# Kernel tuning notes

Hardware: AMD Instinct MI355X
Metric: run time of the kernel (lower is better)

Reference implementation:

```python
import jax, jax.numpy as jnp
import numpy as np

S, P = 64, 32          # scenes, pedestrians per scene (uniform)
N = S * P              # total pedestrians = 2048
H, E = 64, 64          # h_dim, embedding_dim
D1, D2 = 512, 1024     # mlp_pre_pool hidden, bottleneck_dim
EPS = 1e-5             # torch BatchNorm1d eps


def _batchnorm(x, gamma, beta):
    # Training-mode BN with per-scene batch stats (matches the per-scene
    # loop in the original, where BN sees one scene's num_ped^2 rows).
    # x: [S, P*P, D]
    mu = jnp.mean(x, axis=1, keepdims=True)
    var = jnp.mean(jnp.square(x - mu), axis=1, keepdims=True)  # biased var, as torch BN
    return (x - mu) * jax.lax.rsqrt(var + EPS) * gamma + beta


def setup_inputs() -> dict:
    key = jax.random.key(0)
    ks = jax.random.split(key, 16)
    h_states = jax.random.normal(ks[0], (1, N, H), jnp.float32)
    starts = jnp.arange(S, dtype=jnp.int32) * P
    seq_start_end = jnp.stack([starts, starts + P], axis=1)  # [S, 2]
    end_pos = jax.random.normal(ks[1], (N, 2), jnp.float32)
    rel_pos = jax.random.normal(ks[2], (N, 2), jnp.float32)  # unused (pooling_dim=2) but a fwd arg
    sc = 0.05
    params = dict(
        W_embed=jax.random.normal(ks[3], (2, E), jnp.float32) * sc,
        b_embed=jnp.zeros((E,), jnp.float32),
        W1=jax.random.normal(ks[4], (E + H, D1), jnp.float32) * sc,
        b1=jnp.zeros((D1,), jnp.float32),
        g1=jnp.ones((D1,), jnp.float32),
        be1=jnp.zeros((D1,), jnp.float32),
        W2=jax.random.normal(ks[5], (D1, D2), jnp.float32) * sc,
        b2=jnp.zeros((D2,), jnp.float32),
        g2=jnp.ones((D2,), jnp.float32),
        be2=jnp.zeros((D2,), jnp.float32),
    )
    return dict(h_states=h_states, seq_start_end=seq_start_end,
                end_pos=end_pos, rel_pos=rel_pos, **params)


def reference(h_states, seq_start_end, end_pos, rel_pos,
              W_embed, b_embed, W1, b1, g1, be1, W2, b2, g2, be2):
    # Uniform scenes: seq_start_end delimits S contiguous blocks of P peds.
    pos = end_pos.reshape(S, P, 2)
    h = h_states.reshape(N, H).reshape(S, P, H)
    # Original indexing: row (k*P + j) -> pos[j] - pos[k], hidden[j];
    # the final view(P, P, -1).max(1) maxes over j for each k.
    rel = pos[:, None, :, :] - pos[:, :, None, :]          # [S, Pk, Pj, 2]
    emb = rel @ W_embed + b_embed                          # [S, Pk, Pj, E]
    hid = jnp.broadcast_to(h[:, None, :, :], (S, P, P, H)) # hidden of j
    x = jnp.concatenate([emb, hid], axis=-1).reshape(S, P * P, E + H)
    x = jax.nn.relu(_batchnorm(x @ W1 + b1, g1, be1))      # [S, P*P, 512]
    x = jax.nn.relu(_batchnorm(x @ W2 + b2, g2, be2))      # [S, P*P, 1024]
    pool_h = x.reshape(S, P, P, D2).max(axis=2)            # max over j
    return pool_h.reshape(N, D2)
```

## Files before the change

### kernel.cpp

```cpp
#include <hip/hip_runtime.h>
#include <hip/hip_bf16.h>

#define S_ 64
#define P_ 32
#define N_ 2048
#define H_ 64
#define E_ 64
#define D1_ 512
#define D2_ 1024
#define EPS_ 1e-5f

typedef unsigned short u16;
using bf16x8 = __attribute__((ext_vector_type(8))) __bf16;
using floatx4 = __attribute__((ext_vector_type(4))) float;

__device__ inline u16 f2bf(float x) {
    unsigned u = __float_as_uint(x);
    unsigned r = (u + 0x7fffu + ((u >> 16) & 1u)) >> 16;
    return (u16)r;
}


__device__ void prep_scene_256(int u, int tid, float* smem,
                               const float* __restrict__ pos, const float* __restrict__ h,
                               const float* __restrict__ We, const float* __restrict__ W1,
                               const float* __restrict__ g1, const float* __restrict__ be1,
                               float* __restrict__ A, float* __restrict__ Bv) {
    const int s = u >> 2, dq = u & 3;
    const int jg = tid >> 7, dl = tid & 127;
    const int d = (dq << 7) + dl;
    float* hs = smem;
    float* ps = smem + 2048;
    float* red = smem + 2112;
    for (int i = tid; i < 2048; i += 256) hs[i] = h[(size_t)s * 2048 + i];
    if (tid < 64) ps[tid] = pos[s * 64 + tid];
    __syncthreads();
    float wq0 = 0.f, wq1 = 0.f;
    for (int e = 0; e < 64; ++e) {
        const float wv = W1[e * 512 + d];
        wq0 += We[e] * wv;
        wq1 += We[64 + e] * wv;
    }
    float w[16], uu[16];
#pragma unroll
    for (int jj = 0; jj < 16; ++jj) w[jj] = 0.f;
    const float4* h4 = (const float4*)hs;
    for (int e4 = 0; e4 < 16; ++e4) {
        const float c0 = W1[(64 + e4 * 4 + 0) * 512 + d];
        const float c1 = W1[(64 + e4 * 4 + 1) * 512 + d];
        const float c2 = W1[(64 + e4 * 4 + 2) * 512 + d];
        const float c3 = W1[(64 + e4 * 4 + 3) * 512 + d];
#pragma unroll
        for (int jj = 0; jj < 16; ++jj) {
            const float4 hv = h4[((jg << 4) + jj) * 16 + e4];
            w[jj] += hv.x * c0 + hv.y * c1 + hv.z * c2 + hv.w * c3;
        }
    }
    float sw = 0.f, sww = 0.f, su = 0.f, suu = 0.f;
#pragma unroll
    for (int jj = 0; jj < 16; ++jj) {
        const int j = (jg << 4) + jj;
        uu[jj] = ps[2 * j] * wq0 + ps[2 * j + 1] * wq1;
        w[jj] += uu[jj];
        sw += w[jj]; sww += w[jj] * w[jj];
        su += uu[jj]; suu += uu[jj] * uu[jj];
    }
    red[(jg << 7) + dl] = sw;
    red[256 + (jg << 7) + dl] = sww;
    red[512 + (jg << 7) + dl] = su;
    red[768 + (jg << 7) + dl] = suu;
    __syncthreads();
    const float tw = red[dl] + red[128 + dl];
    const float tww = red[256 + dl] + red[384 + dl];
    const float tu = red[512 + dl] + red[640 + dl];
    const float tuu = red[768 + dl] + red[896 + dl];
    const float mw = tw * (1.f / 32.f), mu2 = tu * (1.f / 32.f);
    const float var = (tww * (1.f / 32.f) - mw * mw) + (tuu * (1.f / 32.f) - mu2 * mu2);
    const float sc = rsqrtf(var + EPS_) * g1[d];
    const float bb = be1[d];
#pragma unroll
    for (int jj = 0; jj < 16; ++jj) {
        const int j = (jg << 4) + jj;
        A[(size_t)(s * 32 + j) * 512 + d] = (w[jj] - mw) * sc + bb;
        Bv[(size_t)(s * 32 + j) * 512 + d] = (uu[jj] - mu2) * sc;
    }
}

__device__ void w2t_tile_256(int b2, int tid, void* smem,
                             const float* __restrict__ W2, u16* __restrict__ w2t) {
    float (*tile)[65] = (float (*)[65])smem;
    const int bi = b2 & 15, bj = b2 >> 4;
    const int tx = tid & 63, ty = tid >> 6;
#pragma unroll
    for (int i = 0; i < 64; i += 4)
        tile[ty + i][tx] = W2[(size_t)(bj * 64 + ty + i) * 1024 + bi * 64 + tx];
    __syncthreads();
#pragma unroll
    for (int i = 0; i < 64; i += 4)
        w2t[(size_t)(bi * 64 + ty + i) * 512 + bj * 64 + tx] = f2bf(tile[tx][ty + i]);
}

__global__ __launch_bounds__(256, 2)
void k_gemm(const float* __restrict__ A, const float* __restrict__ Bv,
            const u16* __restrict__ w2t,
            float* __restrict__ maxv, float* __restrict__ minv,
            float* __restrict__ psum, float* __restrict__ psumsq) {
    __shared__ __align__(16) u16 As[128 * 64];
    __shared__ __align__(16) u16 Ws[256 * 64];
    const int tid = threadIdx.x;
    const int wave = tid >> 6, lane = tid & 63;
    const int wm = wave >> 1, wn = wave & 1;
    const int quad = lane >> 4, l16 = lane & 15;
    const int lrow = lane >> 3, lchk = lane & 7;
    const int gchk = lchk ^ lrow;
    const int sj = tid >> 3, sc8 = tid & 7;
    const int mt = blockIdx.x;
    const int s2 = mt >> 3, rb = mt & 7;
    const int pedb = rb << 2;
    const float* Aj = A + ((size_t)(s2 * 32 + sj) << 9) + (sc8 << 3);
    const float* Bp = Bv + ((size_t)(s2 * 32 + pedb) << 9) + (sc8 << 3);
    const int swz = (sc8 ^ (sj & 7)) << 3;

    for (int cs = 0; cs < 4; ++cs) {
        const int N0 = cs << 8;
        floatx4 acc[4][8] = {};
        for (int it = 0; it < 8; ++it) {
            const int k0 = it << 6;
#pragma unroll
            for (int t = 0; t < 8; ++t) {
                const int rbase = (wave << 6) + (t << 3);
                const u16* gb = w2t + (size_t)(N0 + rbase + lrow) * 512 + (k0 + (gchk << 3));
                __builtin_amdgcn_global_load_lds(
                    (const __attribute__((address_space(1))) void*)gb,
                    (__attribute__((address_space(3))) void*)(Ws + (rbase << 6)), 16, 0, 0);
            }
            {
                const float4 alo = *(const float4*)(Aj + k0);
                const float4 ahi = *(const float4*)(Aj + k0 + 4);
#pragma unroll
                for (int p = 0; p < 4; ++p) {
                    const int r = (p << 5) + sj;
                    const float4 blo = *(const float4*)(Bp + ((size_t)p << 9) + k0);
                    const float4 bhi = *(const float4*)(Bp + ((size_t)p << 9) + k0 + 4);
                    bf16x8 o;
                    o[0] = (__bf16)fmaxf(alo.x - blo.x, 0.f);
                    o[1] = (__bf16)fmaxf(alo.y - blo.y, 0.f);
                    o[2] = (__bf16)fmaxf(alo.z - blo.z, 0.f);
                    o[3] = (__bf16)fmaxf(alo.w - blo.w, 0.f);
                    o[4] = (__bf16)fmaxf(ahi.x - bhi.x, 0.f);
                    o[5] = (__bf16)fmaxf(ahi.y - bhi.y, 0.f);
                    o[6] = (__bf16)fmaxf(ahi.z - bhi.z, 0.f);
                    o[7] = (__bf16)fmaxf(ahi.w - bhi.w, 0.f);
                    *(bf16x8*)(As + (r << 6) + swz) = o;
                }
            }
            __syncthreads();
#pragma unroll
            for (int kk = 0; kk < 2; ++kk) {
                const int ck = (kk << 2) + quad;
                const int po = (ck ^ (l16 & 7)) << 3;
                bf16x8 af[4], wf[8];
#pragma unroll
                for (int tm = 0; tm < 4; ++tm) {
                    const int row = (wm << 6) + (tm << 4) + l16;
                    af[tm] = *(const bf16x8*)(As + (row << 6) + po);
                }
#pragma unroll
                for (int tn = 0; tn < 8; ++tn) {
                    const int wrow = (wn << 7) + (tn << 4) + l16;
                    wf[tn] = *(const bf16x8*)(Ws + (wrow << 6) + ((ck ^ (wrow & 7)) << 3));
                }
#pragma unroll
                for (int tm = 0; tm < 4; ++tm)
#pragma unroll
                    for (int tn = 0; tn < 8; ++tn)
                        acc[tm][tn] = __builtin_amdgcn_mfma_f32_16x16x32_bf16(
                            af[tm], wf[tn], acc[tm][tn], 0, 0, 0);
            }
            __syncthreads();
        }
#pragma unroll
        for (int tn = 0; tn < 8; ++tn) {
            const int col = N0 + (wn << 7) + (tn << 4) + l16;
            float wsum = 0.f, wsq = 0.f;
#pragma unroll
            for (int gp = 0; gp < 2; ++gp) {
                float vmax = -3.4e38f, vmin = 3.4e38f, vs = 0.f, vq = 0.f;
#pragma unroll
                for (int tm = gp * 2; tm < gp * 2 + 2; ++tm)
#pragma unroll
                    for (int r = 0; r < 4; ++r) {
                        const float v = acc[tm][tn][r];
                        vmax = fmaxf(vmax, v);
                        vmin = fminf(vmin, v);
                        vs += v;
                        vq += v * v;
                    }
#pragma unroll
                for (int off = 16; off < 64; off <<= 1) {
                    vmax = fmaxf(vmax, __shfl_xor(vmax, off));
                    vmin = fminf(vmin, __shfl_xor(vmin, off));
                    vs += __shfl_xor(vs, off);
                    vq += __shfl_xor(vq, off);
                }
                if (quad == 0) {
                    const int kg = s2 * 32 + pedb + (wm << 1) + gp;
                    maxv[(size_t)kg * 1024 + col] = vmax;
                    minv[(size_t)kg * 1024 + col] = vmin;
                }
                wsum += vs;
                wsq += vq;
            }
            if (quad == 0) {
                const int slot = (s2 << 4) + (rb << 1) + wm;
                psum[(size_t)slot * 1024 + col] = wsum;
                psumsq[(size_t)slot * 1024 + col] = wsq;
            }
        }
    }
}

__global__ __launch_bounds__(256)
void k_prep(const float* __restrict__ pos, const float* __restrict__ h,
            const float* __restrict__ We, const float* __restrict__ W1,
            const float* __restrict__ g1, const float* __restrict__ be1,
            const float* __restrict__ W2,
            float* __restrict__ A, float* __restrict__ Bv, u16* __restrict__ w2t) {
    __shared__ __align__(16) char smem_raw[16912];
    const int bid = blockIdx.x;
    if (bid < 256)
        prep_scene_256(bid, threadIdx.x, (float*)smem_raw, pos, h, We, W1, g1, be1, A, Bv);
    else
        w2t_tile_256(bid - 256, threadIdx.x, smem_raw, W2, w2t);
}

__global__ __launch_bounds__(256)
void k_final(const float* __restrict__ maxv, const float* __restrict__ minv,
             const float* __restrict__ psum, const float* __restrict__ psumsq,
             const float* __restrict__ g2, const float* __restrict__ be2,
             float* __restrict__ out) {
    const int u = blockIdx.x, tid = threadIdx.x;
    const int s3 = u >> 2;
    const int c = ((u & 3) << 8) + tid;
    float sm = 0.f, sq = 0.f;
#pragma unroll
    for (int t = 0; t < 16; ++t) {
        sm += psum[(size_t)(s3 * 16 + t) * 1024 + c];
        sq += psumsq[(size_t)(s3 * 16 + t) * 1024 + c];
    }
    const float mu = sm * (1.f / 1024.f);
    const float var = sq * (1.f / 1024.f) - mu * mu;
    const float inv = rsqrtf(var + EPS_);
    const float scale = g2[c] * inv;
    const float bb = be2[c];
    const float* src = (scale >= 0.f) ? maxv : minv;
    for (int k = 0; k < 32; ++k) {
        const float v = src[(size_t)(s3 * 32 + k) * 1024 + c];
        out[(size_t)(s3 * 32 + k) * 1024 + c] = fmaxf((v - mu) * scale + bb, 0.f);
    }
}

extern "C" void kernel_launch(void* const* d_in, const int* in_sizes, int n_in,
                              void* d_out, int out_size, void* d_ws, size_t ws_size,
                              hipStream_t stream) {
    const float* h_states = (const float*)d_in[0];
    const float* end_pos = (const float*)d_in[2];
    const float* W_embed = (const float*)d_in[4];
    const float* W1 = (const float*)d_in[6];
    const float* g1 = (const float*)d_in[8];
    const float* be1 = (const float*)d_in[9];
    const float* W2 = (const float*)d_in[10];
    const float* g2 = (const float*)d_in[12];
    const float* be2 = (const float*)d_in[13];
    float* out = (float*)d_out;

    float* Abuf = (float*)d_ws;
    float* Bbuf = Abuf + 1048576;
    float* maxv = Bbuf + 1048576;
    float* minv = maxv + 2097152;
    float* psum = minv + 2097152;
    float* psumsq = psum + 1048576;
    u16* w2t = (u16*)(psumsq + 1048576);

    k_prep<<<dim3(384), dim3(256), 0, stream>>>(end_pos, h_states, W_embed, W1,
                                                g1, be1, W2, Abuf, Bbuf, w2t);
    k_gemm<<<dim3(512), dim3(256), 0, stream>>>(Abuf, Bbuf, w2t, maxv, minv, psum, psumsq);
    k_final<<<dim3(256), dim3(256), 0, stream>>>(maxv, minv, psum, psumsq, g2, be2, out);
}
```

Before: 183.9 us.

## Fuse BN2 finalize into GEMM kernel via per-scene last-block counter

Removes the separate k_final launch. Each GEMM block bumps an atomic per-scene counter, and the last of the 8 blocks for a scene reduces the partial sums, applies BN and ReLU, and writes the output. The partial stores become agent-scope atomics so the last block sees them, and a memset is added to reset the counters. The B-tile loads are also hoisted ahead of the conversion loop. In exchange, the tail work is serialized onto the last block of each scene and an extra memset is issued.

```diff
diff --git a/kernel.cpp b/kernel.cpp
--- a/kernel.cpp
+++ b/kernel.cpp
@@ -19,7 +19,6 @@
     unsigned r = (u + 0x7fffu + ((u >> 16) & 1u)) >> 16;
     return (u16)r;
 }
-
 
 __device__ void prep_scene_256(int u, int tid, float* smem,
                                const float* __restrict__ pos, const float* __restrict__ h,
@@ -100,13 +99,31 @@
         w2t[(size_t)(bi * 64 + ty + i) * 512 + bj * 64 + tx] = f2bf(tile[tx][ty + i]);
 }
 
+__global__ __launch_bounds__(256)
+void k_prep(const float* __restrict__ pos, const float* __restrict__ h,
+            const float* __restrict__ We, const float* __restrict__ W1,
+            const float* __restrict__ g1, const float* __restrict__ be1,
+            const float* __restrict__ W2,
+            float* __restrict__ A, float* __restrict__ Bv, u16* __restrict__ w2t) {
+    __shared__ __align__(16) char smem_raw[16912];
+    const int bid = blockIdx.x;
+    if (bid < 256)
+        prep_scene_256(bid, threadIdx.x, (float*)smem_raw, pos, h, We, W1, g1, be1, A, Bv);
+    else
+        w2t_tile_256(bid - 256, threadIdx.x, smem_raw, W2, w2t);
+}
+
 __global__ __launch_bounds__(256, 2)
 void k_gemm(const float* __restrict__ A, const float* __restrict__ Bv,
             const u16* __restrict__ w2t,
             float* __restrict__ maxv, float* __restrict__ minv,
-            float* __restrict__ psum, float* __restrict__ psumsq) {
+            float* __restrict__ psum, float* __restrict__ psumsq,
+            int* __restrict__ cnt,
+            const float* __restrict__ g2, const float* __restrict__ be2,
+            float* __restrict__ out) {
     __shared__ __align__(16) u16 As[128 * 64];
     __shared__ __align__(16) u16 Ws[256 * 64];
+    __shared__ int last_flag;
     const int tid = threadIdx.x;
     const int wave = tid >> 6, lane = tid & 63;
     const int wm = wave >> 1, wn = wave & 1;
@@ -135,22 +152,26 @@
                     (__attribute__((address_space(3))) void*)(Ws + (rbase << 6)), 16, 0, 0);
             }
             {
-                const float4 alo = *(const float4*)(Aj + k0);
-                const float4 ahi = *(const float4*)(Aj + k0 + 4);
+                const float4 a0 = *(const float4*)(Aj + k0);
+                const float4 a1 = *(const float4*)(Aj + k0 + 4);
+                float4 bl[4], bh[4];
+#pragma unroll
+                for (int p = 0; p < 4; ++p) {
+                    bl[p] = *(const float4*)(Bp + ((size_t)p << 9) + k0);
+                    bh[p] = *(const float4*)(Bp + ((size_t)p << 9) + k0 + 4);
+                }
 #pragma unroll
                 for (int p = 0; p < 4; ++p) {
                     const int r = (p << 5) + sj;
-                    const float4 blo = *(const float4*)(Bp + ((size_t)p << 9) + k0);
-                    const float4 bhi = *(const float4*)(Bp + ((size_t)p << 9) + k0 + 4);
                     bf16x8 o;
-                    o[0] = (__bf16)fmaxf(alo.x - blo.x, 0.f);
-                    o[1] = (__bf16)fmaxf(alo.y - blo.y, 0.f);
-                    o[2] = (__bf16)fmaxf(alo.z - blo.z, 0.f);
-                    o[3] = (__bf16)fmaxf(alo.w - blo.w, 0.f);
-                    o[4] = (__bf16)fmaxf(ahi.x - bhi.x, 0.f);
-                    o[5] = (__bf16)fmaxf(ahi.y - bhi.y, 0.f);
-                    o[6] = (__bf16)fmaxf(ahi.z - bhi.z, 0.f);
-                    o[7] = (__bf16)fmaxf(ahi.w - bhi.w, 0.f);
+                    o[0] = (__bf16)fmaxf(a0.x - bl[p].x, 0.f);
+                    o[1] = (__bf16)fmaxf(a0.y - bl[p].y, 0.f);
+                    o[2] = (__bf16)fmaxf(a0.z - bl[p].z, 0.f);
+                    o[3] = (__bf16)fmaxf(a0.w - bl[p].w, 0.f);
+                    o[4] = (__bf16)fmaxf(a1.x - bh[p].x, 0.f);
+                    o[5] = (__bf16)fmaxf(a1.y - bh[p].y, 0.f);
+                    o[6] = (__bf16)fmaxf(a1.z - bh[p].z, 0.f);
+                    o[7] = (__bf16)fmaxf(a1.w - bh[p].w, 0.f);
                     *(bf16x8*)(As + (r << 6) + swz) = o;
                 }
             }
@@ -205,58 +226,51 @@
                 }
                 if (quad == 0) {
                     const int kg = s2 * 32 + pedb + (wm << 1) + gp;
-                    maxv[(size_t)kg * 1024 + col] = vmax;
-                    minv[(size_t)kg * 1024 + col] = vmin;
+                    __hip_atomic_store(&maxv[(size_t)kg * 1024 + col], vmax,
+                                       __ATOMIC_RELAXED, __HIP_MEMORY_SCOPE_AGENT);
+                    __hip_atomic_store(&minv[(size_t)kg * 1024 + col], vmin,
+                                       __ATOMIC_RELAXED, __HIP_MEMORY_SCOPE_AGENT);
                 }
                 wsum += vs;
                 wsq += vq;
             }
             if (quad == 0) {
                 const int slot = (s2 << 4) + (rb << 1) + wm;
-                psum[(size_t)slot * 1024 + col] = wsum;
-                psumsq[(size_t)slot * 1024 + col] = wsq;
+                __hip_atomic_store(&psum[(size_t)slot * 1024 + col], wsum,
+                                   __ATOMIC_RELAXED, __HIP_MEMORY_SCOPE_AGENT);
+                __hip_atomic_store(&psumsq[(size_t)slot * 1024 + col], wsq,
+                                   __ATOMIC_RELAXED, __HIP_MEMORY_SCOPE_AGENT);
             }
         }
     }
-}
-
-__global__ __launch_bounds__(256)
-void k_prep(const float* __restrict__ pos, const float* __restrict__ h,
-            const float* __restrict__ We, const float* __restrict__ W1,
-            const float* __restrict__ g1, const float* __restrict__ be1,
-            const float* __restrict__ W2,
-            float* __restrict__ A, float* __restrict__ Bv, u16* __restrict__ w2t) {
-    __shared__ __align__(16) char smem_raw[16912];
-    const int bid = blockIdx.x;
-    if (bid < 256)
-        prep_scene_256(bid, threadIdx.x, (float*)smem_raw, pos, h, We, W1, g1, be1, A, Bv);
-    else
-        w2t_tile_256(bid - 256, threadIdx.x, smem_raw, W2, w2t);
-}
-
-__global__ __launch_bounds__(256)
-void k_final(const float* __restrict__ maxv, const float* __restrict__ minv,
-             const float* __restrict__ psum, const float* __restrict__ psumsq,
-             const float* __restrict__ g2, const float* __restrict__ be2,
-             float* __restrict__ out) {
-    const int u = blockIdx.x, tid = threadIdx.x;
-    const int s3 = u >> 2;
-    const int c = ((u & 3) << 8) + tid;
-    float sm = 0.f, sq = 0.f;
-#pragma unroll
-    for (int t = 0; t < 16; ++t) {
-        sm += psum[(size_t)(s3 * 16 + t) * 1024 + c];
-        sq += psumsq[(size_t)(s3 * 16 + t) * 1024 + c];
-    }
-    const float mu = sm * (1.f / 1024.f);
-    const float var = sq * (1.f / 1024.f) - mu * mu;
-    const float inv = rsqrtf(var + EPS_);
-    const float scale = g2[c] * inv;
-    const float bb = be2[c];
-    const float* src = (scale >= 0.f) ? maxv : minv;
-    for (int k = 0; k < 32; ++k) {
-        const float v = src[(size_t)(s3 * 32 + k) * 1024 + c];
-        out[(size_t)(s3 * 32 + k) * 1024 + c] = fmaxf((v - mu) * scale + bb, 0.f);
+
+    __syncthreads();
+    if (tid == 0) {
+        const int old = __hip_atomic_fetch_add(&cnt[s2], 1,
+                                               __ATOMIC_ACQ_REL, __HIP_MEMORY_SCOPE_AGENT);
+        last_flag = (old == 7);
+    }
+    __syncthreads();
+    if (last_flag) {
+#pragma unroll
+        for (int q = 0; q < 4; ++q) {
+            const int c = (q << 8) + tid;
+            float sm = 0.f, sq = 0.f;
+#pragma unroll
+            for (int t = 0; t < 16; ++t) {
+                sm += psum[(size_t)(s2 * 16 + t) * 1024 + c];
+                sq += psumsq[(size_t)(s2 * 16 + t) * 1024 + c];
+            }
+            const float mu = sm * (1.f / 1024.f);
+            const float var = sq * (1.f / 1024.f) - mu * mu;
+            const float scale = g2[c] * rsqrtf(var + EPS_);
+            const float bb = be2[c];
+            const float* src = (scale >= 0.f) ? maxv : minv;
+            for (int k = 0; k < 32; ++k) {
+                const float v = src[(size_t)(s2 * 32 + k) * 1024 + c];
+                out[(size_t)(s2 * 32 + k) * 1024 + c] = fmaxf((v - mu) * scale + bb, 0.f);
+            }
+        }
     }
 }
 
@@ -281,9 +295,11 @@
     float* psum = minv + 2097152;
     float* psumsq = psum + 1048576;
     u16* w2t = (u16*)(psumsq + 1048576);
-
+    int* cnt = (int*)(w2t + 524288);
+
+    hipMemsetAsync(cnt, 0, 64 * sizeof(int), stream);
     k_prep<<<dim3(384), dim3(256), 0, stream>>>(end_pos, h_states, W_embed, W1,
                                                 g1, be1, W2, Abuf, Bbuf, w2t);
-    k_gemm<<<dim3(512), dim3(256), 0, stream>>>(Abuf, Bbuf, w2t, maxv, minv, psum, psumsq);
-    k_final<<<dim3(256), dim3(256), 0, stream>>>(maxv, minv, psum, psumsq, g2, be2, out);
-}
+    k_gemm<<<dim3(512), dim3(256), 0, stream>>>(Abuf, Bbuf, w2t, maxv, minv,
+                                                psum, psumsq, cnt, g2, be2, out);
+}
```

Result: slower. 202.5 us (+10.1%).
